# Kernel optimization log

Measured on AMD Instinct MI355X. Metric: run time of the kernel, lower is better.

The kernel has to match this reference:

```python
import jax, jax.numpy as jnp
import numpy as np

E = 2048
H = 16
DH = E // H  # 128
B, T = 2, 2048
EPS = 1e-8


def rmsnorm(x, g):
    rms = jnp.sqrt(jnp.mean(x * x, axis=-1, keepdims=True) + EPS)
    return g * (x / rms)


def setup_inputs() -> dict:
    key = jax.random.key(0)
    ks = jax.random.split(key, 16)
    s_in = 1.0 / np.sqrt(E)
    s_ff = 1.0 / np.sqrt(4 * E)
    return {
        "x": jax.random.normal(ks[0], (B, T, E), dtype=jnp.float32),
        # stacked per-head QKV projections, stored (in, out) so y = x @ W + b
        "wq": jax.random.normal(ks[1], (H, E, DH), dtype=jnp.float32) * s_in,
        "bq": jax.random.normal(ks[2], (H, DH), dtype=jnp.float32) * s_in,
        "wk": jax.random.normal(ks[3], (H, E, DH), dtype=jnp.float32) * s_in,
        "bk": jax.random.normal(ks[4], (H, DH), dtype=jnp.float32) * s_in,
        "wv": jax.random.normal(ks[5], (H, E, DH), dtype=jnp.float32) * s_in,
        "bv": jax.random.normal(ks[6], (H, DH), dtype=jnp.float32) * s_in,
        "wo": jax.random.normal(ks[7], (E, E), dtype=jnp.float32) * s_in,
        "bo": jax.random.normal(ks[8], (E,), dtype=jnp.float32) * s_in,
        "w1": jax.random.normal(ks[9], (E, 4 * E), dtype=jnp.float32) * s_in,
        "b1": jax.random.normal(ks[10], (4 * E,), dtype=jnp.float32) * s_in,
        "w2": jax.random.normal(ks[11], (4 * E, E), dtype=jnp.float32) * s_ff,
        "b2": jax.random.normal(ks[12], (E,), dtype=jnp.float32) * s_ff,
        "g1": jnp.ones((E,), dtype=jnp.float32),
        "g2": jnp.ones((E,), dtype=jnp.float32),
    }


def reference(x, wq, bq, wk, bk, wv, bv, wo, bo, w1, b1, w2, b2, g1, g2):
    b, t, e = x.shape
    # --- attention sublayer ---
    h = rmsnorm(x, g1)
    q = jnp.einsum("bte,hed->bhtd", h, wq) + bq[None, :, None, :]
    k = jnp.einsum("bte,hed->bhtd", h, wk) + bk[None, :, None, :]
    v = jnp.einsum("bte,hed->bhtd", h, wv) + bv[None, :, None, :]
    scores = jnp.einsum("bhtd,bhsd->bhts", q, k) / jnp.sqrt(jnp.float32(DH))
    causal = jnp.tril(jnp.ones((t, t), dtype=bool))
    scores = jnp.where(causal[None, None], scores, -jnp.inf)
    w = jax.nn.softmax(scores, axis=-1)
    o = jnp.einsum("bhts,bhsd->bhtd", w, v)
    o = o.transpose(0, 2, 1, 3).reshape(b, t, e)  # concat heads on last dim
    x = x + o @ wo + bo
    # --- FFN sublayer (exact GELU, dropout is identity at inference) ---
    h = rmsnorm(x, g2)
    x = x + jax.nn.gelu(h @ w1 + b1, approximate=False) @ w2 + b2
    return x
```

## Files before the change

### kernel.cpp

```cpp
#include <hip/hip_runtime.h>
#include <hip/hip_bf16.h>

typedef unsigned short u16;
typedef unsigned int   u32;
typedef __attribute__((ext_vector_type(8))) short short8;
typedef __attribute__((ext_vector_type(4))) float f32x4;
typedef __attribute__((ext_vector_type(4))) unsigned short u16x4;

#define E_    2048
#define H_    16
#define DH_   128
#define B_    2
#define T_    2048
#define NTOK  4096
#define QKVN  6144

#define VMCNT(n) asm volatile("s_waitcnt vmcnt(" #n ")" ::: "memory")
#define LGKM0()  asm volatile("s_waitcnt lgkmcnt(0)" ::: "memory")

__device__ __forceinline__ u16 f2bf(float f) {
  union { float f; u32 u; } v; v.f = f;
  u32 r = (v.u + 0x7FFFu + ((v.u >> 16) & 1u)) >> 16;
  return (u16)r;
}

__device__ __forceinline__ void tr64_body(
    const float* __restrict__ ib, u16* __restrict__ ob,
    int R, int C, int r0, int c0, int tid, float (*t)[65])
{
  const int rr = tid >> 4;
  const int cc = (tid & 15) * 4;
  #pragma unroll
  for (int p = 0; p < 4; ++p) {
    const float4 v = *(const float4*)(ib + (size_t)(r0 + p * 16 + rr) * C + c0 + cc);
    t[cc + 0][p * 16 + rr] = v.x;
    t[cc + 1][p * 16 + rr] = v.y;
    t[cc + 2][p * 16 + rr] = v.z;
    t[cc + 3][p * 16 + rr] = v.w;
  }
  __syncthreads();
  const int wr = tid >> 3;
  const int wc = (tid & 7) * 8;
  #pragma unroll
  for (int p = 0; p < 2; ++p) {
    short8 s;
    #pragma unroll
    for (int j = 0; j < 8; ++j) s[j] = (short)f2bf(t[p * 32 + wr][wc + j]);
    *(short8*)(ob + (size_t)(c0 + p * 32 + wr) * R + r0 + wc) = s;
  }
}

__device__ __forceinline__ void rms_body(
    const float* __restrict__ x, const float* __restrict__ g,
    u16* __restrict__ o, int row, int tid, float* wsum)
{
  const float4* xr = (const float4*)(x + (size_t)row * E_);
  const float4* gr = (const float4*)g;
  float4 a0 = xr[tid], a1 = xr[tid + 256];
  float s = a0.x*a0.x + a0.y*a0.y + a0.z*a0.z + a0.w*a0.w
          + a1.x*a1.x + a1.y*a1.y + a1.z*a1.z + a1.w*a1.w;
  #pragma unroll
  for (int m = 1; m < 64; m <<= 1) s += __shfl_xor(s, m);
  if ((tid & 63) == 0) wsum[tid >> 6] = s;
  __syncthreads();
  float tot = wsum[0] + wsum[1] + wsum[2] + wsum[3];
  float rinv = rsqrtf(tot * (1.0f / E_) + 1e-8f);
  float4 g0 = gr[tid], g1v = gr[tid + 256];
  u16x4 o0, o1;
  o0[0] = f2bf(a0.x * g0.x * rinv); o0[1] = f2bf(a0.y * g0.y * rinv);
  o0[2] = f2bf(a0.z * g0.z * rinv); o0[3] = f2bf(a0.w * g0.w * rinv);
  o1[0] = f2bf(a1.x * g1v.x * rinv); o1[1] = f2bf(a1.y * g1v.y * rinv);
  o1[2] = f2bf(a1.z * g1v.z * rinv); o1[3] = f2bf(a1.w * g1v.w * rinv);
  u16x4* orow = (u16x4*)(o + (size_t)row * E_);
  orow[tid] = o0;
  orow[tid + 256] = o1;
}

__global__ __launch_bounds__(256) void prep_all(
    const float* __restrict__ wq, const float* __restrict__ wk, const float* __restrict__ wv,
    const float* __restrict__ wo, const float* __restrict__ w1, const float* __restrict__ w2,
    const float* __restrict__ bq, const float* __restrict__ bk, const float* __restrict__ bv,
    u16* __restrict__ wqkv_t, u16* __restrict__ wo_t, u16* __restrict__ w1_t, u16* __restrict__ w2_t,
    float* __restrict__ bqkv,
    const float* __restrict__ x, const float* __restrict__ g1, u16* __restrict__ h1)
{
  __shared__ float t[64][65];
  const int bid = blockIdx.x;
  const int tid = threadIdx.x;
  if (bid < 3072) {
    const int sec = bid >> 10;
    const int tI  = bid & 1023;
    const int z   = tI >> 6;
    const int by  = (tI >> 1) & 31;
    const int bx  = tI & 1;
    const float* src = (sec == 0) ? wq : (sec == 1) ? wk : wv;
    tr64_body(src + (size_t)z * E_ * DH_,
              wqkv_t + (size_t)sec * E_ * E_ + (size_t)z * DH_ * E_,
              E_, DH_, by * 64, bx * 64, tid, t);
  } else if (bid < 4096) {
    const int tI = bid - 3072;
    tr64_body(wo, wo_t, E_, E_, (tI >> 5) * 64, (tI & 31) * 64, tid, t);
  } else if (bid < 8192) {
    const int tI = bid - 4096;
    tr64_body(w1, w1_t, E_, 4 * E_, (tI >> 7) * 64, (tI & 127) * 64, tid, t);
  } else if (bid < 12288) {
    const int tI = bid - 8192;
    tr64_body(w2, w2_t, 4 * E_, E_, (tI >> 5) * 64, (tI & 31) * 64, tid, t);
  } else if (bid < 12312) {
    const int idx = (bid - 12288) * 256 + tid;
    const float* bb = (idx < 2048) ? bq : (idx < 4096) ? bk : bv;
    bqkv[idx] = bb[idx & 2047];
  } else {
    rms_body(x, g1, h1, bid - 12312, tid, &t[0][0]);
  }
}

__global__ __launch_bounds__(256) void rmsnorm_k(
    const float* __restrict__ x, const float* __restrict__ g, u16* __restrict__ o)
{
  __shared__ float wsum[4];
  rms_body(x, g, o, blockIdx.x, threadIdx.x, wsum);
}

__device__ __forceinline__ void gload_lds16(const void* g, u16* lds_base) {
  __builtin_amdgcn_global_load_lds(
      (const __attribute__((address_space(1))) u32*)g,
      (__attribute__((address_space(3))) u32*)lds_base, 16, 0, 0);
}

template<int BM, int BN, int MODE, int EPI>
__global__ __launch_bounds__(512, 2)
void gemm3(const u16* __restrict__ A, const u16* __restrict__ Bt,
           const float* __restrict__ bias, const float* __restrict__ resid,
           void* __restrict__ out, u16* __restrict__ vtout, int M, int N, int K)
{
  constexpr int WROWS = BM / 2;
  constexpr int WCOLS = BN / 4;
  constexpr int MR    = WROWS / 16;
  constexpr int BUF   = (BM + BN) * 32;
  __shared__ __align__(16) u16 sh[3 * BUF];

  const int tid  = threadIdx.x;
  const int lane = tid & 63;
  const int l15  = lane & 15, lg = lane >> 4;
  const int w    = tid >> 6;
  const int wm   = w >> 2;
  const int wn   = w & 3;
  const int xs   = (l15 >> 1) & 3;

  const int nbx = N / BN;
  const int xcd = blockIdx.x & 7, j = blockIdx.x >> 3;
  int m0, n0;
  if constexpr (MODE == 1) {
    const int ncx = nbx >> 3;
    n0 = (xcd * ncx + j % ncx) * BN;
    m0 = (j / ncx) * BM;
  } else {
    const int nwg = nbx * (M / BM);
    const int sid = xcd * (nwg >> 3) + j;
    m0 = (sid / nbx) * BM;
    n0 = (sid % nbx) * BN;
  }

  const int r0 = tid >> 2;
  const int c0 = (((tid & 3) ^ ((tid >> 3) & 3)) * 8);
  const u16* gA  = A  + (size_t)(m0 + r0) * K + c0;
  const u16* gB  = Bt + (size_t)(n0 + r0) * K + c0;
  const u16* gA2 = gA + (size_t)128 * K;
  const u16* gB2 = gB + (size_t)128 * K;
  const int wub = (tid & ~63) * 8;

  f32x4 acc[MR][4] = {};
  const int NT = K >> 5;

  #pragma unroll
  for (int t = 0; t < 2; ++t) {
    u16* wb = sh + t * BUF;
    const int kS = t * 32;
    if constexpr (BM == 256) {
      gload_lds16(gA  + kS, wb + wub);
      gload_lds16(gA2 + kS, wb + 4096 + wub);
      gload_lds16(gB  + kS, wb + 8192 + wub);
      gload_lds16(gB2 + kS, wb + 12288 + wub);
    } else {
      gload_lds16(gA  + kS, wb + wub);
      gload_lds16(gB  + kS, wb + 4096 + wub);
      gload_lds16(gB2 + kS, wb + 8192 + wub);
    }
  }
  if constexpr (BM == 256) VMCNT(4); else VMCNT(3);
  __builtin_amdgcn_s_barrier();

  int i = 0;

#define KTILE(CUR, STG)                                                          \
  do {                                                                           \
    const u16* rb = sh + (CUR) * BUF;                                            \
    u16* wb = sh + (STG) * BUF;                                                  \
    const bool st = (i + 2 < NT);                                                \
    const int kS = (i + 2) << 5;                                                 \
    const int rem = NT - 1 - i;                                                  \
    if (st) {                                                                    \
      if constexpr (BM == 256) {                                                 \
        gload_lds16(gA  + kS, wb + wub);                                         \
        gload_lds16(gA2 + kS, wb + 4096 + wub);                                  \
        gload_lds16(gB  + kS, wb + 8192 + wub);                                  \
        gload_lds16(gB2 + kS, wb + 12288 + wub);                                 \
      } else {                                                                   \
        gload_lds16(gA  + kS, wb + wub);                                         \
        gload_lds16(gB  + kS, wb + 4096 + wub);                                  \
        gload_lds16(gB2 + kS, wb + 8192 + wub);                                  \
      }                                                                          \
    }                                                                            \
    short8 bf[4];                                                                \
    _Pragma("unroll")                                                            \
    for (int n = 0; n < 4; ++n)                                                  \
      bf[n] = *(const short8*)(rb + BM * 32 + (wn * WCOLS + n * 16 + l15) * 32 + ((lg ^ xs) * 8)); \
    _Pragma("unroll")                                                            \
    for (int mh = 0; mh < MR / 4; ++mh) {                                        \
      short8 af[4];                                                              \
      _Pragma("unroll")                                                          \
      for (int m = 0; m < 4; ++m)                                                \
        af[m] = *(const short8*)(rb + (wm * WROWS + (mh * 4 + m) * 16 + l15) * 32 + ((lg ^ xs) * 8)); \
      _Pragma("unroll")                                                          \
      for (int m = 0; m < 4; ++m)                                                \
        _Pragma("unroll")                                                        \
        for (int n = 0; n < 4; ++n)                                              \
          acc[mh * 4 + m][n] = __builtin_amdgcn_mfma_f32_16x16x32_bf16(af[m], bf[n], acc[mh * 4 + m][n], 0, 0, 0); \
    }                                                                            \
    if (rem >= 2) { if constexpr (BM == 256) { VMCNT(4); } else { VMCNT(3); } }  \
    else { VMCNT(0); }                                                           \
    __builtin_amdgcn_s_barrier();                                                \
    ++i;                                                                         \
  } while (0)

  const int trips = NT / 3;
  #pragma unroll 1
  for (int t = 0; t < trips; ++t) {
    KTILE(0, 2);
    KTILE(1, 0);
    KTILE(2, 1);
  }
  if (i < NT) KTILE(0, 2);
  if (i < NT) KTILE(1, 0);
#undef KTILE

  float bv[4];
  #pragma unroll
  for (int n = 0; n < 4; ++n) bv[n] = bias[n0 + wn * WCOLS + n * 16 + l15];

  if constexpr (EPI == 1) {
    #pragma unroll
    for (int n = 0; n < 4; ++n) {
      const int col = n0 + wn * WCOLS + n * 16 + l15;
      #pragma unroll
      for (int m = 0; m < MR; ++m)
        #pragma unroll
        for (int r = 0; r < 4; ++r) {
          const int row = m0 + wm * WROWS + m * 16 + lg * 4 + r;
          const size_t off = (size_t)row * N + col;
          ((float*)out)[off] = acc[m][n][r] + bv[n] + resid[off];
        }
    }
  } else if (EPI == 3 && n0 >= 4096) {
    u16* epb = sh + w * 4096;
    const int colV0 = n0 - 4096 + wn * 64;
    const int hh = colV0 >> 7;
    const int db = colV0 & 127;
    const int tw = m0 + wm * WROWS;
    const int bb = tw >> 11;
    const int tb = tw & 2047;
    u16* vbase = vtout + ((size_t)(bb * 16 + hh) * 128 + db) * 2048 + tb;
    #pragma unroll
    for (int mh = 0; mh < MR / 4; ++mh) {
      #pragma unroll
      for (int n = 0; n < 4; ++n)
        #pragma unroll
        for (int mm = 0; mm < 4; ++mm)
          #pragma unroll
          for (int r = 0; r < 4; ++r)
            epb[(n * 16 + l15) * 64 + mm * 16 + lg * 4 + r] =
                f2bf(acc[mh * 4 + mm][n][r] + bv[n]);
      LGKM0();
      #pragma unroll
      for (int it = 0; it < 8; ++it) {
        const int c = it * 64 + lane;
        const int d = c >> 3, sl = c & 7;
        short8 s = *(const short8*)(epb + d * 64 + sl * 8);
        *(short8*)(vbase + (size_t)d * 2048 + mh * 64 + sl * 8) = s;
      }
      LGKM0();
    }
  } else {
    u16* ep = sh + w * 1024;
    #pragma unroll
    for (int m = 0; m < MR; ++m) {
      #pragma unroll
      for (int n = 0; n < 4; ++n)
        #pragma unroll
        for (int r = 0; r < 4; ++r) {
          float v = acc[m][n][r] + bv[n];
          if (EPI == 2) {
            float t = v * (0.79788456080286536f + 0.0356774081363231f * v * v);
            v = v / (1.0f + __expf(-2.0f * t));
          }
          ep[(lg * 4 + r) * 64 + n * 16 + l15] = f2bf(v);
        }
      LGKM0();
      const int row0 = m0 + wm * WROWS + m * 16;
      #pragma unroll
      for (int it = 0; it < 2; ++it) {
        const int ch = it * 64 + lane;
        const int rr = ch >> 3, c8 = ch & 7;
        short8 s = *(const short8*)(ep + rr * 64 + c8 * 8);
        *(short8*)((u16*)out + (size_t)(row0 + rr) * N + n0 + wn * WCOLS + c8 * 8) = s;
      }
      LGKM0();
    }
  }
}

__global__ __launch_bounds__(256) void attn_k(
    const u16* __restrict__ qkv, const u16* __restrict__ vt, u16* __restrict__ o)
{
  const int tid  = threadIdx.x;
  const int lane = tid & 63;
  const int w    = tid >> 6;
  const int l15  = lane & 15, lg = lane >> 4;
  const int bid  = blockIdx.x;
  const int pair = bid & 31;
  const int qt   = 15 - (bid >> 5);
  const int h    = pair & 15;
  const int b    = pair >> 4;
  const int Q0 = qt * 128;
  const int qw = Q0 + w * 32;

  __shared__ __align__(16) u16 Ks[2][64 * 128];
  __shared__ __align__(16) u16 Vs[2][128 * 64];
  __shared__ __align__(16) u16 Ps[4][32 * 64];

  const u16* qb  = qkv + (size_t)b * T_ * QKVN + h * DH_;
  const u16* kb  = qb + E_;
  const u16* vtb = vt + (size_t)(b * H_ + h) * DH_ * T_;

  short8 qf[2][4];
  #pragma unroll
  for (int qi = 0; qi < 2; ++qi)
    #pragma unroll
    for (int kk = 0; kk < 4; ++kk)
      qf[qi][kk] = *(const short8*)(qb + (size_t)(qw + qi * 16 + l15) * QKVN + kk * 32 + lg * 8);

  f32x4 oacc[2][8] = {};
  float m_[2][4], l_[2][4];
  #pragma unroll
  for (int qi = 0; qi < 2; ++qi)
    #pragma unroll
    for (int r = 0; r < 4; ++r) { m_[qi][r] = -1e30f; l_[qi][r] = 0.f; }

  const int xr = l15 & 7;
  const float scl = 0.08838834764831845f;
  const int nt = Q0 / 64 + 2;
  const int qmaxw = qw + 31;
  const int wub = (tid & ~63);

  const u16* kp[4]; const u16* vp[4];
  #pragma unroll
  for (int i = 0; i < 4; ++i) {
    int f = i * 256 + tid;
    int r = f >> 4, p = f & 15, c = p ^ (r & 7);
    kp[i] = kb + (size_t)r * QKVN + c * 8;
  }
  #pragma unroll
  for (int i = 0; i < 4; ++i) {
    int f = i * 256 + tid;
    int d = f >> 3, p = f & 7, c = p ^ (d & 7);
    vp[i] = vtb + (size_t)d * T_ + c * 8;
  }

  auto STAGEKV = [&](int s0, int bufi) {
    const size_t ko = (size_t)s0 * QKVN;
    #pragma unroll
    for (int i = 0; i < 4; ++i)
      gload_lds16(kp[i] + ko, &Ks[bufi][(i * 256 + wub) * 8]);
    #pragma unroll
    for (int i = 0; i < 4; ++i)
      gload_lds16(vp[i] + s0, &Vs[bufi][(i * 256 + wub) * 8]);
  };

  STAGEKV(0, 0);
  VMCNT(0);
  __builtin_amdgcn_s_barrier();

  #pragma unroll 1
  for (int st = 0; st < nt; ++st) {
    const int s0 = st * 64;
    const int cur = st & 1;
    if (st + 1 < nt) STAGEKV(s0 + 64, cur ^ 1);

    if (s0 <= qmaxw) {
      const u16* Kc = Ks[cur];
      const u16* Vc = Vs[cur];
      f32x4 sc[2][4] = {};
      __builtin_amdgcn_s_setprio(1);
      #pragma unroll
      for (int sj = 0; sj < 4; ++sj) {
        const int row = sj * 16 + l15;
        #pragma unroll
        for (int kk = 0; kk < 4; ++kk) {
          short8 kfr = *(const short8*)(Kc + row * 128 + (((kk * 4 + lg) ^ xr) * 8));
          sc[0][sj] = __builtin_amdgcn_mfma_f32_16x16x32_bf16(qf[0][kk], kfr, sc[0][sj], 0, 0, 0);
          sc[1][sj] = __builtin_amdgcn_mfma_f32_16x16x32_bf16(qf[1][kk], kfr, sc[1][sj], 0, 0, 0);
        }
      }
      __builtin_amdgcn_s_setprio(0);
      const bool needmask = (s0 + 63 > qw);
      #pragma unroll
      for (int qi = 0; qi < 2; ++qi)
        #pragma unroll
        for (int sj = 0; sj < 4; ++sj)
          #pragma unroll
          for (int r = 0; r < 4; ++r) {
            float v = sc[qi][sj][r] * scl;
            if (needmask) {
              int s = s0 + sj * 16 + l15;
              int q = qw + qi * 16 + lg * 4 + r;
              if (s > q) v = -1e30f;
            }
            sc[qi][sj][r] = v;
          }
      float tmax[2][4];
      #pragma unroll
      for (int qi = 0; qi < 2; ++qi) {
        #pragma unroll
        for (int r = 0; r < 4; ++r) {
          tmax[qi][r] = fmaxf(fmaxf(sc[qi][0][r], sc[qi][1][r]), fmaxf(sc[qi][2][r], sc[qi][3][r]));
          #pragma unroll
          for (int m = 1; m < 16; m <<= 1) tmax[qi][r] = fmaxf(tmax[qi][r], __shfl_xor(tmax[qi][r], m));
        }
      }
      bool grow = false;
      #pragma unroll
      for (int qi = 0; qi < 2; ++qi)
        #pragma unroll
        for (int r = 0; r < 4; ++r) grow |= (tmax[qi][r] > m_[qi][r] + 8.0f);
      if (__any(grow)) {
        #pragma unroll
        for (int qi = 0; qi < 2; ++qi) {
          float alpha[4];
          #pragma unroll
          for (int r = 0; r < 4; ++r) {
            float mn = fmaxf(m_[qi][r], tmax[qi][r]);
            alpha[r] = __expf(m_[qi][r] - mn);
            m_[qi][r] = mn;
            l_[qi][r] *= alpha[r];
          }
          #pragma unroll
          for (int dj = 0; dj < 8; ++dj)
            #pragma unroll
            for (int r = 0; r < 4; ++r) oacc[qi][dj][r] *= alpha[r];
        }
      }
      #pragma unroll
      for (int qi = 0; qi < 2; ++qi) {
        float rsum[4] = {0.f, 0.f, 0.f, 0.f};
        #pragma unroll
        for (int sj = 0; sj < 4; ++sj)
          #pragma unroll
          for (int r = 0; r < 4; ++r) {
            float p = __expf(sc[qi][sj][r] - m_[qi][r]);
            rsum[r] += p;
            const int row = qi * 16 + lg * 4 + r;
            const int ch  = (sj * 2 + (l15 >> 3)) ^ (row & 7);
            Ps[w][row * 64 + ch * 8 + (l15 & 7)] = f2bf(p);
          }
        #pragma unroll
        for (int r = 0; r < 4; ++r) {
          #pragma unroll
          for (int m = 1; m < 16; m <<= 1) rsum[r] += __shfl_xor(rsum[r], m);
          l_[qi][r] += rsum[r];
        }
      }
      __builtin_amdgcn_s_setprio(1);
      #pragma unroll
      for (int ks = 0; ks < 2; ++ks) {
        short8 pf0 = *(const short8*)(&Ps[w][l15 * 64 + (((ks * 4 + lg) ^ xr) * 8)]);
        short8 pf1 = *(const short8*)(&Ps[w][(16 + l15) * 64 + (((ks * 4 + lg) ^ xr) * 8)]);
        #pragma unroll
        for (int dj = 0; dj < 8; ++dj) {
          const int row = dj * 16 + l15;
          short8 vfr = *(const short8*)(Vc + row * 64 + (((ks * 4 + lg) ^ xr) * 8));
          oacc[0][dj] = __builtin_amdgcn_mfma_f32_16x16x32_bf16(pf0, vfr, oacc[0][dj], 0, 0, 0);
          oacc[1][dj] = __builtin_amdgcn_mfma_f32_16x16x32_bf16(pf1, vfr, oacc[1][dj], 0, 0, 0);
        }
      }
      __builtin_amdgcn_s_setprio(0);
    }
    VMCNT(0);
    __builtin_amdgcn_s_barrier();
  }

  float inv[2][4];
  #pragma unroll
  for (int qi = 0; qi < 2; ++qi)
    #pragma unroll
    for (int r = 0; r < 4; ++r) inv[qi][r] = 1.0f / l_[qi][r];
  u16* ob = o + (size_t)(b * T_ + qw) * E_ + h * DH_;
  #pragma unroll
  for (int qi = 0; qi < 2; ++qi)
    #pragma unroll
    for (int dj = 0; dj < 8; ++dj)
      #pragma unroll
      for (int r = 0; r < 4; ++r)
        ob[(size_t)(qi * 16 + lg * 4 + r) * E_ + dj * 16 + l15] = f2bf(oacc[qi][dj][r] * inv[qi][r]);
}

extern "C" void kernel_launch(void* const* d_in, const int* in_sizes, int n_in,
                              void* d_out, int out_size, void* d_ws, size_t ws_size,
                              hipStream_t stream)
{
  const float* x  = (const float*)d_in[0];
  const float* wq = (const float*)d_in[1];
  const float* bq = (const float*)d_in[2];
  const float* wk = (const float*)d_in[3];
  const float* bk = (const float*)d_in[4];
  const float* wv = (const float*)d_in[5];
  const float* bv = (const float*)d_in[6];
  const float* wo = (const float*)d_in[7];
  const float* bo = (const float*)d_in[8];
  const float* w1 = (const float*)d_in[9];
  const float* b1 = (const float*)d_in[10];
  const float* w2 = (const float*)d_in[11];
  const float* b2 = (const float*)d_in[12];
  const float* g1 = (const float*)d_in[13];
  const float* g2 = (const float*)d_in[14];
  float* xout = (float*)d_out;

  if (ws_size < 201351168u) return;

  char* ws = (char*)d_ws;
  u16*   wqkv_t = (u16*)(ws + 0);
  u16*   h1     = (u16*)(ws + 25165824);
  u16*   qkv    = (u16*)(ws + 41943040);
  u16*   vt     = (u16*)(ws + 92274688);
  u16*   o_     = (u16*)(ws + 109051904);
  u16*   wo_t   = (u16*)(ws + 125829120);
  u16*   w1_t   = (u16*)(ws + 134217728);
  u16*   w2_t   = (u16*)(ws + 167772160);
  float* bqkv   = (float*)(ws + 201326592);
  u16*   u_     = (u16*)(ws + 0);
  u16*   h2     = vt;
  float* x2     = xout;

  prep_all<<<12312 + 4096, 256, 0, stream>>>(wq, wk, wv, wo, w1, w2, bq, bk, bv,
                                             wqkv_t, wo_t, w1_t, w2_t, bqkv,
                                             x, g1, h1);

  gemm3<128, 256, 1, 3><<<(NTOK / 128) * (QKVN / 256), 512, 0, stream>>>(h1, wqkv_t, bqkv, nullptr, qkv, vt, NTOK, QKVN, E_);
  attn_k<<<B_ * H_ * (T_ / 16 / 8), 256, 0, stream>>>(qkv, vt, o_);
  gemm3<128, 256, 0, 1><<<(NTOK / 128) * (E_ / 256), 512, 0, stream>>>(o_, wo_t, bo, x, x2, nullptr, NTOK, E_, E_);
  rmsnorm_k<<<NTOK, 256, 0, stream>>>(x2, g2, h2);
  gemm3<256, 256, 1, 2><<<(NTOK / 256) * (4 * E_ / 256), 512, 0, stream>>>(h2, w1_t, b1, nullptr, u_, nullptr, NTOK, 4 * E_, E_);
  gemm3<128, 256, 0, 1><<<(NTOK / 128) * (E_ / 256), 512, 0, stream>>>(u_, w2_t, b2, x2, xout, nullptr, NTOK, E_, 4 * E_);
}
```

Measured before the change: 654.8 us.

## Read K/V fragments directly from global memory in attention, drop LDS staging

The attention kernel stops staging K and V tiles through double-buffered shared memory with block-wide barriers. Each wave now loads its MFMA K and V^T fragments straight from global memory and loops only over the key tiles its own 32 queries need, removing the block synchronisation. This cuts LDS traffic, barriers and causally unneeded work per wave. In exchange the four waves each fetch the same K/V data separately through cache, and global load latency is no longer hidden by the prefetch of the next tile.

```diff
diff --git a/kernel.cpp b/kernel.cpp
--- a/kernel.cpp
+++ b/kernel.cpp
@@ -335,8 +335,6 @@
   const int Q0 = qt * 128;
   const int qw = Q0 + w * 32;
 
-  __shared__ __align__(16) u16 Ks[2][64 * 128];
-  __shared__ __align__(16) u16 Vs[2][128 * 64];
   __shared__ __align__(16) u16 Ps[4][32 * 64];
 
   const u16* qb  = qkv + (size_t)b * T_ * QKVN + h * DH_;
@@ -357,146 +355,112 @@
     #pragma unroll
     for (int r = 0; r < 4; ++r) { m_[qi][r] = -1e30f; l_[qi][r] = 0.f; }
 
-  const int xr = l15 & 7;
   const float scl = 0.08838834764831845f;
-  const int nt = Q0 / 64 + 2;
   const int qmaxw = qw + 31;
-  const int wub = (tid & ~63);
-
-  const u16* kp[4]; const u16* vp[4];
-  #pragma unroll
-  for (int i = 0; i < 4; ++i) {
-    int f = i * 256 + tid;
-    int r = f >> 4, p = f & 15, c = p ^ (r & 7);
-    kp[i] = kb + (size_t)r * QKVN + c * 8;
-  }
-  #pragma unroll
-  for (int i = 0; i < 4; ++i) {
-    int f = i * 256 + tid;
-    int d = f >> 3, p = f & 7, c = p ^ (d & 7);
-    vp[i] = vtb + (size_t)d * T_ + c * 8;
-  }
-
-  auto STAGEKV = [&](int s0, int bufi) {
-    const size_t ko = (size_t)s0 * QKVN;
-    #pragma unroll
-    for (int i = 0; i < 4; ++i)
-      gload_lds16(kp[i] + ko, &Ks[bufi][(i * 256 + wub) * 8]);
-    #pragma unroll
-    for (int i = 0; i < 4; ++i)
-      gload_lds16(vp[i] + s0, &Vs[bufi][(i * 256 + wub) * 8]);
-  };
-
-  STAGEKV(0, 0);
-  VMCNT(0);
-  __builtin_amdgcn_s_barrier();
+  const int ntw = (qmaxw >> 6) + 1;
 
   #pragma unroll 1
-  for (int st = 0; st < nt; ++st) {
+  for (int st = 0; st < ntw; ++st) {
     const int s0 = st * 64;
-    const int cur = st & 1;
-    if (st + 1 < nt) STAGEKV(s0 + 64, cur ^ 1);
-
-    if (s0 <= qmaxw) {
-      const u16* Kc = Ks[cur];
-      const u16* Vc = Vs[cur];
-      f32x4 sc[2][4] = {};
-      __builtin_amdgcn_s_setprio(1);
-      #pragma unroll
-      for (int sj = 0; sj < 4; ++sj) {
-        const int row = sj * 16 + l15;
-        #pragma unroll
-        for (int kk = 0; kk < 4; ++kk) {
-          short8 kfr = *(const short8*)(Kc + row * 128 + (((kk * 4 + lg) ^ xr) * 8));
-          sc[0][sj] = __builtin_amdgcn_mfma_f32_16x16x32_bf16(qf[0][kk], kfr, sc[0][sj], 0, 0, 0);
-          sc[1][sj] = __builtin_amdgcn_mfma_f32_16x16x32_bf16(qf[1][kk], kfr, sc[1][sj], 0, 0, 0);
+    f32x4 sc[2][4] = {};
+    __builtin_amdgcn_s_setprio(1);
+    #pragma unroll
+    for (int sj = 0; sj < 4; ++sj) {
+      const u16* kr = kb + (size_t)(s0 + sj * 16 + l15) * QKVN + lg * 8;
+      #pragma unroll
+      for (int kk = 0; kk < 4; ++kk) {
+        short8 kfr = *(const short8*)(kr + kk * 32);
+        sc[0][sj] = __builtin_amdgcn_mfma_f32_16x16x32_bf16(qf[0][kk], kfr, sc[0][sj], 0, 0, 0);
+        sc[1][sj] = __builtin_amdgcn_mfma_f32_16x16x32_bf16(qf[1][kk], kfr, sc[1][sj], 0, 0, 0);
+      }
+    }
+    __builtin_amdgcn_s_setprio(0);
+    const bool needmask = (s0 + 63 > qw);
+    #pragma unroll
+    for (int qi = 0; qi < 2; ++qi)
+      #pragma unroll
+      for (int sj = 0; sj < 4; ++sj)
+        #pragma unroll
+        for (int r = 0; r < 4; ++r) {
+          float v = sc[qi][sj][r] * scl;
+          if (needmask) {
+            int s = s0 + sj * 16 + l15;
+            int q = qw + qi * 16 + lg * 4 + r;
+            if (s > q) v = -1e30f;
+          }
+          sc[qi][sj][r] = v;
         }
-      }
-      __builtin_amdgcn_s_setprio(0);
-      const bool needmask = (s0 + 63 > qw);
-      #pragma unroll
-      for (int qi = 0; qi < 2; ++qi)
-        #pragma unroll
-        for (int sj = 0; sj < 4; ++sj)
+    float tmax[2][4];
+    #pragma unroll
+    for (int qi = 0; qi < 2; ++qi) {
+      #pragma unroll
+      for (int r = 0; r < 4; ++r) {
+        tmax[qi][r] = fmaxf(fmaxf(sc[qi][0][r], sc[qi][1][r]), fmaxf(sc[qi][2][r], sc[qi][3][r]));
+        #pragma unroll
+        for (int m = 1; m < 16; m <<= 1) tmax[qi][r] = fmaxf(tmax[qi][r], __shfl_xor(tmax[qi][r], m));
+      }
+    }
+    bool grow = false;
+    #pragma unroll
+    for (int qi = 0; qi < 2; ++qi)
+      #pragma unroll
+      for (int r = 0; r < 4; ++r) grow |= (tmax[qi][r] > m_[qi][r] + 8.0f);
+    if (__any(grow)) {
+      #pragma unroll
+      for (int qi = 0; qi < 2; ++qi) {
+        float alpha[4];
+        #pragma unroll
+        for (int r = 0; r < 4; ++r) {
+          float mn = fmaxf(m_[qi][r], tmax[qi][r]);
+          alpha[r] = __expf(m_[qi][r] - mn);
+          m_[qi][r] = mn;
+          l_[qi][r] *= alpha[r];
+        }
+        #pragma unroll
+        for (int dj = 0; dj < 8; ++dj)
           #pragma unroll
-          for (int r = 0; r < 4; ++r) {
-            float v = sc[qi][sj][r] * scl;
-            if (needmask) {
-              int s = s0 + sj * 16 + l15;
-              int q = qw + qi * 16 + lg * 4 + r;
-              if (s > q) v = -1e30f;
-            }
-            sc[qi][sj][r] = v;
-          }
-      float tmax[2][4];
-      #pragma unroll
-      for (int qi = 0; qi < 2; ++qi) {
+          for (int r = 0; r < 4; ++r) oacc[qi][dj][r] *= alpha[r];
+      }
+    }
+    #pragma unroll
+    for (int qi = 0; qi < 2; ++qi) {
+      float rsum[4] = {0.f, 0.f, 0.f, 0.f};
+      #pragma unroll
+      for (int sj = 0; sj < 4; ++sj)
         #pragma unroll
         for (int r = 0; r < 4; ++r) {
-          tmax[qi][r] = fmaxf(fmaxf(sc[qi][0][r], sc[qi][1][r]), fmaxf(sc[qi][2][r], sc[qi][3][r]));
-          #pragma unroll
-          for (int m = 1; m < 16; m <<= 1) tmax[qi][r] = fmaxf(tmax[qi][r], __shfl_xor(tmax[qi][r], m));
+          float p = __expf(sc[qi][sj][r] - m_[qi][r]);
+          rsum[r] += p;
+          const int row = qi * 16 + lg * 4 + r;
+          const int ch  = (sj * 2 + (l15 >> 3)) ^ (row & 7);
+          Ps[w][row * 64 + ch * 8 + (l15 & 7)] = f2bf(p);
         }
-      }
-      bool grow = false;
-      #pragma unroll
-      for (int qi = 0; qi < 2; ++qi)
-        #pragma unroll
-        for (int r = 0; r < 4; ++r) grow |= (tmax[qi][r] > m_[qi][r] + 8.0f);
-      if (__any(grow)) {
-        #pragma unroll
-        for (int qi = 0; qi < 2; ++qi) {
-          float alpha[4];
-          #pragma unroll
-          for (int r = 0; r < 4; ++r) {
-            float mn = fmaxf(m_[qi][r], tmax[qi][r]);
-            alpha[r] = __expf(m_[qi][r] - mn);
-            m_[qi][r] = mn;
-            l_[qi][r] *= alpha[r];
-          }
-          #pragma unroll
-          for (int dj = 0; dj < 8; ++dj)
-            #pragma unroll
-            for (int r = 0; r < 4; ++r) oacc[qi][dj][r] *= alpha[r];
-        }
-      }
-      #pragma unroll
-      for (int qi = 0; qi < 2; ++qi) {
-        float rsum[4] = {0.f, 0.f, 0.f, 0.f};
-        #pragma unroll
-        for (int sj = 0; sj < 4; ++sj)
-          #pragma unroll
-          for (int r = 0; r < 4; ++r) {
-            float p = __expf(sc[qi][sj][r] - m_[qi][r]);
-            rsum[r] += p;
-            const int row = qi * 16 + lg * 4 + r;
-            const int ch  = (sj * 2 + (l15 >> 3)) ^ (row & 7);
-            Ps[w][row * 64 + ch * 8 + (l15 & 7)] = f2bf(p);
-          }
-        #pragma unroll
-        for (int r = 0; r < 4; ++r) {
-          #pragma unroll
-          for (int m = 1; m < 16; m <<= 1) rsum[r] += __shfl_xor(rsum[r], m);
-          l_[qi][r] += rsum[r];
-        }
-      }
-      __builtin_amdgcn_s_setprio(1);
-      #pragma unroll
-      for (int ks = 0; ks < 2; ++ks) {
-        short8 pf0 = *(const short8*)(&Ps[w][l15 * 64 + (((ks * 4 + lg) ^ xr) * 8)]);
-        short8 pf1 = *(const short8*)(&Ps[w][(16 + l15) * 64 + (((ks * 4 + lg) ^ xr) * 8)]);
-        #pragma unroll
-        for (int dj = 0; dj < 8; ++dj) {
-          const int row = dj * 16 + l15;
-          short8 vfr = *(const short8*)(Vc + row * 64 + (((ks * 4 + lg) ^ xr) * 8));
-          oacc[0][dj] = __builtin_amdgcn_mfma_f32_16x16x32_bf16(pf0, vfr, oacc[0][dj], 0, 0, 0);
-          oacc[1][dj] = __builtin_amdgcn_mfma_f32_16x16x32_bf16(pf1, vfr, oacc[1][dj], 0, 0, 0);
-        }
-      }
-      __builtin_amdgcn_s_setprio(0);
-    }
-    VMCNT(0);
-    __builtin_amdgcn_s_barrier();
+      #pragma unroll
+      for (int r = 0; r < 4; ++r) {
+        #pragma unroll
+        for (int m = 1; m < 16; m <<= 1) rsum[r] += __shfl_xor(rsum[r], m);
+        l_[qi][r] += rsum[r];
+      }
+    }
+    LGKM0();
+    __builtin_amdgcn_sched_barrier(0);
+    __builtin_amdgcn_s_setprio(1);
+    const int xr = l15 & 7;
+    #pragma unroll
+    for (int ks = 0; ks < 2; ++ks) {
+      short8 pf0 = *(const short8*)(&Ps[w][l15 * 64 + (((ks * 4 + lg) ^ xr) * 8)]);
+      short8 pf1 = *(const short8*)(&Ps[w][(16 + l15) * 64 + (((ks * 4 + lg) ^ xr) * 8)]);
+      #pragma unroll
+      for (int dj = 0; dj < 8; ++dj) {
+        const u16* vr = vtb + (size_t)(dj * 16 + l15) * T_ + s0 + ks * 32 + lg * 8;
+        short8 vfr = *(const short8*)vr;
+        oacc[0][dj] = __builtin_amdgcn_mfma_f32_16x16x32_bf16(pf0, vfr, oacc[0][dj], 0, 0, 0);
+        oacc[1][dj] = __builtin_amdgcn_mfma_f32_16x16x32_bf16(pf1, vfr, oacc[1][dj], 0, 0, 0);
+      }
+    }
+    __builtin_amdgcn_s_setprio(0);
+    LGKM0();
+    __builtin_amdgcn_sched_barrier(0);
   }
 
   float inv[2][4];
```

New measurement: 738.6 us. 12.8% more time.
